# Kernel tuning notes

Hardware: AMD Instinct MI355X
Metric: run time of the kernel (lower is better)

Reference implementation:

```python
import jax, jax.numpy as jnp
import numpy as np
import math

N, CIN, COUT, H, W, K = 8, 192, 192, 64, 64, 1024


def setup_inputs() -> dict:
    key = jax.random.key(0)
    k1, k2, k3, k4, k5 = jax.random.split(key, 5)
    latent = jax.random.normal(k1, (N, CIN, H, W), dtype=jnp.float32)
    # kaiming-uniform-like codebook init
    bound = math.sqrt(6.0 / COUT)
    codebook = jax.random.uniform(k2, (K, COUT), dtype=jnp.float32, minval=-bound, maxval=bound)
    # nn.Linear weights: [out_features, in_features]
    wq = jax.random.normal(k3, (COUT, CIN), dtype=jnp.float32) / math.sqrt(CIN)
    wk = jax.random.normal(k4, (COUT, COUT), dtype=jnp.float32) / math.sqrt(COUT)
    wv = jax.random.normal(k5, (COUT, COUT), dtype=jnp.float32) / math.sqrt(COUT)
    temperature1 = jnp.ones((), dtype=jnp.float32)
    return {"latent": latent, "codebook": codebook, "wq": wq, "wk": wk, "wv": wv,
            "temperature1": temperature1, "temperature": 1}


def reference(latent, codebook, wq, wk, wv, temperature1, temperature):
    # latent: [n, cin, h, w] -> q: [n, h, w, cout]
    q = jnp.einsum('nchw,oc->nhwo', latent, wq)
    k = codebook @ wk.T          # [K, cout]
    v = codebook @ wv.T          # [K, cout]
    scale = math.sqrt(CIN)
    # logit: [n, h, w, K]
    logit = jnp.einsum('nhwd,kd->nhwk', q, k) / scale * temperature1
    trueCode = jnp.argmax(logit, axis=-1)  # [n, h, w]
    # gumbel-softmax, hard=True (straight-through)
    gumbel = jax.random.gumbel(jax.random.key(42), logit.shape, dtype=logit.dtype)
    y_soft = jax.nn.softmax((logit + gumbel) / temperature, axis=-1)
    idx = jnp.argmax(y_soft, axis=-1)
    y_hard = jax.nn.one_hot(idx, K, dtype=logit.dtype)
    sample = y_hard + y_soft - jax.lax.stop_gradient(y_soft)
    # quantized: [n, h, w, cout] -> [n, cout, h, w]
    quantized = jnp.einsum('nhwk,kd->nhwd', sample, v).transpose(0, 3, 1, 2)
    return quantized, trueCode, logit
```

## Files before the change

kernel.cpp:

```cpp
#include <hip/hip_runtime.h>
#include <cstdint>
#include <cstddef>

#define CIN   192
#define COUT  192
#define KCB   1024
#define HWSZ  4096
#define NPIX  32768
#define LOGIT_SCALE_F 13.856406460551018f

#define QCOL0 832

__device__ __forceinline__ void threefry_0_42(uint32_t x0, uint32_t x1,
                                              uint32_t& o0, uint32_t& o1) {
  const uint32_t ks0 = 0u;
  const uint32_t ks1 = 42u;
  const uint32_t ks2 = 0x1BD11BDAu ^ 0u ^ 42u;
  x0 += ks0; x1 += ks1;
#define TFR(r) { x0 += x1; x1 = (x1 << (r)) | (x1 >> (32 - (r))); x1 ^= x0; }
  TFR(13) TFR(15) TFR(26) TFR(6)
  x0 += ks1; x1 += ks2 + 1u;
  TFR(17) TFR(29) TFR(16) TFR(24)
  x0 += ks2; x1 += ks0 + 2u;
  TFR(13) TFR(15) TFR(26) TFR(6)
  x0 += ks0; x1 += ks1 + 3u;
  TFR(17) TFR(29) TFR(16) TFR(24)
  x0 += ks1; x1 += ks2 + 4u;
  TFR(13) TFR(15) TFR(26) TFR(6)
  x0 += ks2; x1 += ks0 + 5u;
#undef TFR
  o0 = x0; o1 = x1;
}

__device__ __forceinline__ float gumbel_from_bits(uint32_t b) {
  float u = __uint_as_float((b >> 9) | 0x3F800000u) - 1.0f;
  u = fmaxf(u, 1.17549435e-38f);
  return -logf(-logf(u));
}

#define FMA16(acc, av, bv) do { \
  acc[0][0]=fmaf(av.x,bv.x,acc[0][0]); acc[0][1]=fmaf(av.x,bv.y,acc[0][1]); \
  acc[0][2]=fmaf(av.x,bv.z,acc[0][2]); acc[0][3]=fmaf(av.x,bv.w,acc[0][3]); \
  acc[1][0]=fmaf(av.y,bv.x,acc[1][0]); acc[1][1]=fmaf(av.y,bv.y,acc[1][1]); \
  acc[1][2]=fmaf(av.y,bv.z,acc[1][2]); acc[1][3]=fmaf(av.y,bv.w,acc[1][3]); \
  acc[2][0]=fmaf(av.z,bv.x,acc[2][0]); acc[2][1]=fmaf(av.z,bv.y,acc[2][1]); \
  acc[2][2]=fmaf(av.z,bv.z,acc[2][2]); acc[2][3]=fmaf(av.z,bv.w,acc[2][3]); \
  acc[3][0]=fmaf(av.w,bv.x,acc[3][0]); acc[3][1]=fmaf(av.w,bv.y,acc[3][1]); \
  acc[3][2]=fmaf(av.w,bv.z,acc[3][2]); acc[3][3]=fmaf(av.w,bv.w,acc[3][3]); \
} while (0)

#define FMA8(accr, a, b0, b1) do { \
  accr[0]=fmaf(a,b0.x,accr[0]); accr[1]=fmaf(a,b0.y,accr[1]); \
  accr[2]=fmaf(a,b0.z,accr[2]); accr[3]=fmaf(a,b0.w,accr[3]); \
  accr[4]=fmaf(a,b1.x,accr[4]); accr[5]=fmaf(a,b1.y,accr[5]); \
  accr[6]=fmaf(a,b1.z,accr[6]); accr[7]=fmaf(a,b1.w,accr[7]); \
} while (0)

__global__ __launch_bounds__(256) void kv_kernel(
    const float* __restrict__ cb, const float* __restrict__ wk,
    const float* __restrict__ wv, float* __restrict__ km, float* __restrict__ vm) {
  __shared__ float sCb[32][68];
  __shared__ float sK[32][68];
  __shared__ float sV[32][68];
  const int tid = threadIdx.x;
  const int j0 = blockIdx.x * 64;
  const int o0 = blockIdx.y * 64;
  const float4* cb4 = reinterpret_cast<const float4*>(cb);
  const float4* wk4 = reinterpret_cast<const float4*>(wk);
  const float4* wv4 = reinterpret_cast<const float4*>(wv);
  const int c4 = tid & 7, rr = tid >> 3;
  const int tp = tid & 15, to = tid >> 4;
  float ak[4][4] = {};
  float av_[4][4] = {};

  for (int ci = 0; ci < 6; ++ci) {
    __syncthreads();
    {
      const int cf = ci * 8 + c4;
#pragma unroll
      for (int pass = 0; pass < 2; ++pass) {
        const int r = rr + pass * 32;
        float4 a = cb4[(size_t)(j0 + r) * 48 + cf];
        float4 b = wk4[(size_t)(o0 + r) * 48 + cf];
        float4 c = wv4[(size_t)(o0 + r) * 48 + cf];
        sCb[4 * c4 + 0][r] = a.x; sCb[4 * c4 + 1][r] = a.y;
        sCb[4 * c4 + 2][r] = a.z; sCb[4 * c4 + 3][r] = a.w;
        sK[4 * c4 + 0][r] = b.x; sK[4 * c4 + 1][r] = b.y;
        sK[4 * c4 + 2][r] = b.z; sK[4 * c4 + 3][r] = b.w;
        sV[4 * c4 + 0][r] = c.x; sV[4 * c4 + 1][r] = c.y;
        sV[4 * c4 + 2][r] = c.z; sV[4 * c4 + 3][r] = c.w;
      }
    }
    __syncthreads();
#pragma unroll
    for (int c = 0; c < 32; ++c) {
      float4 a = *reinterpret_cast<const float4*>(&sCb[c][4 * tp]);
      float4 bk = *reinterpret_cast<const float4*>(&sK[c][4 * to]);
      float4 bv = *reinterpret_cast<const float4*>(&sV[c][4 * to]);
      FMA16(ak, a, bk);
      FMA16(av_, a, bv);
    }
  }
#pragma unroll
  for (int ii = 0; ii < 4; ++ii) {
    float4 w;
    w.x = ak[ii][0]; w.y = ak[ii][1]; w.z = ak[ii][2]; w.w = ak[ii][3];
    *reinterpret_cast<float4*>(km + (size_t)(j0 + 4 * tp + ii) * COUT + o0 + 4 * to) = w;
    float4 v;
    v.x = av_[ii][0]; v.y = av_[ii][1]; v.z = av_[ii][2]; v.w = av_[ii][3];
    *reinterpret_cast<float4*>(vm + (size_t)(j0 + 4 * tp + ii) * COUT + o0 + 4 * to) = v;
  }
}

__global__ __launch_bounds__(256) void q_kernel(
    const float* __restrict__ latent, const float* __restrict__ wq,
    float* __restrict__ logitq) {
  __shared__ float sA[32][68];
  __shared__ float sB[32][68];
  const int tid = threadIdx.x;
  const int p0 = blockIdx.x * 64;
  const int o0 = blockIdx.y * 64;
  const int n = p0 >> 12, hw0 = p0 & 4095;
  const float4* lat4 =
      reinterpret_cast<const float4*>(latent + (size_t)n * (CIN * HWSZ));
  const float4* wq4 = reinterpret_cast<const float4*>(wq);
  const int hw40 = hw0 >> 2;
  const int lf = tid & 15, lr = tid >> 4;
  const int wc4 = tid & 7, wr = tid >> 3;
  const int tp = tid & 15, to = tid >> 4;
  float acc[4][4] = {};

  for (int ci = 0; ci < 6; ++ci) {
    const int c0 = ci * 32;
    __syncthreads();
    {
      float4 l0 = lat4[(size_t)(c0 + lr) * (HWSZ / 4) + hw40 + lf];
      float4 l1 = lat4[(size_t)(c0 + lr + 16) * (HWSZ / 4) + hw40 + lf];
      float4 w0 = wq4[(size_t)(o0 + wr) * 48 + (c0 >> 2) + wc4];
      float4 w1 = wq4[(size_t)(o0 + wr + 32) * 48 + (c0 >> 2) + wc4];
      *reinterpret_cast<float4*>(&sA[lr][4 * lf]) = l0;
      *reinterpret_cast<float4*>(&sA[lr + 16][4 * lf]) = l1;
      sB[4 * wc4 + 0][wr] = w0.x; sB[4 * wc4 + 1][wr] = w0.y;
      sB[4 * wc4 + 2][wr] = w0.z; sB[4 * wc4 + 3][wr] = w0.w;
      sB[4 * wc4 + 0][wr + 32] = w1.x; sB[4 * wc4 + 1][wr + 32] = w1.y;
      sB[4 * wc4 + 2][wr + 32] = w1.z; sB[4 * wc4 + 3][wr + 32] = w1.w;
    }
    __syncthreads();
#pragma unroll
    for (int c = 0; c < 32; ++c) {
      float4 av = *reinterpret_cast<const float4*>(&sA[c][4 * tp]);
      float4 bv = *reinterpret_cast<const float4*>(&sB[c][4 * to]);
      FMA16(acc, av, bv);
    }
  }
#pragma unroll
  for (int ii = 0; ii < 4; ++ii) {
    float4 w;
    w.x = acc[ii][0]; w.y = acc[ii][1]; w.z = acc[ii][2]; w.w = acc[ii][3];
    *reinterpret_cast<float4*>(
        logitq + (size_t)(p0 + 4 * tp + ii) * KCB + QCOL0 + o0 + 4 * to) = w;
  }
}

__global__ __launch_bounds__(256) void logit_kernel(
    const float* __restrict__ km, const float* __restrict__ vm,
    const float* __restrict__ t1p, float* __restrict__ logit_out,
    float* __restrict__ code_out, float* __restrict__ quant_out) {
  __shared__ float aT[CIN][36];
  __shared__ float bT[32][132];
  __shared__ float wLv[32][4];
  __shared__ int   wLi[32][4];
  __shared__ float wSv[32][4];
  __shared__ int   wSi[32][4];
  __shared__ int   sIdx[32];

  const int tid = threadIdx.x;
  const int p0 = blockIdx.x * 32;
  const float t1 = t1p[0];

  for (int i = 0; i < 6; ++i) {
    int flat = tid + i * 256;
    int r = flat / 48, c4 = flat % 48;
    float4 v = reinterpret_cast<const float4*>(
        logit_out + (size_t)(p0 + r) * KCB + QCOL0)[c4];
    aT[c4 * 4 + 0][r] = v.x;
    aT[c4 * 4 + 1][r] = v.y;
    aT[c4 * 4 + 2][r] = v.z;
    aT[c4 * 4 + 3][r] = v.w;
  }

  const int tp = tid & 15;
  const int to = tid >> 4;
  float Lv[2], Sv[2];
  int Li[2], Si[2];
#pragma unroll
  for (int ii = 0; ii < 2; ++ii) {
    Lv[ii] = -INFINITY; Sv[ii] = -INFINITY; Li[ii] = 0; Si[ii] = 0;
  }

  const float4* km4 = reinterpret_cast<const float4*>(km);
  const int sc4 = tid & 7, sjj = tid >> 3;

  for (int jt = 0; jt < 8; ++jt) {
    float acc[2][8] = {};
    for (int ci = 0; ci < 6; ++ci) {
      const int c0 = ci * 32;
      __syncthreads();
      {
#pragma unroll
        for (int pass = 0; pass < 4; ++pass) {
          const int jloc = sjj + pass * 32;
          const int jg = jt * 128 + jloc;
          float4 v = km4[(size_t)jg * 48 + (c0 >> 2) + sc4];
          bT[4 * sc4 + 0][jloc] = v.x; bT[4 * sc4 + 1][jloc] = v.y;
          bT[4 * sc4 + 2][jloc] = v.z; bT[4 * sc4 + 3][jloc] = v.w;
        }
      }
      __syncthreads();
#pragma unroll
      for (int c = 0; c < 32; ++c) {
        float2 a2 = *reinterpret_cast<const float2*>(&aT[c0 + c][2 * tp]);
        float4 b0 = *reinterpret_cast<const float4*>(&bT[c][8 * to]);
        float4 b1 = *reinterpret_cast<const float4*>(&bT[c][8 * to + 4]);
        FMA8(acc[0], a2.x, b0, b1);
        FMA8(acc[1], a2.y, b0, b1);
      }
    }
#pragma unroll
    for (int ii = 0; ii < 2; ++ii) {
      const int p = p0 + 2 * tp + ii;
      const int jb = jt * 128 + 8 * to;
      float lv[8];
#pragma unroll
      for (int k = 0; k < 8; ++k) lv[k] = acc[ii][k] / LOGIT_SCALE_F * t1;
      float4 w0, w1;
      w0.x = lv[0]; w0.y = lv[1]; w0.z = lv[2]; w0.w = lv[3];
      w1.x = lv[4]; w1.y = lv[5]; w1.z = lv[6]; w1.w = lv[7];
      float* lrow = logit_out + (size_t)p * KCB + jb;
      *reinterpret_cast<float4*>(lrow) = w0;
      *reinterpret_cast<float4*>(lrow + 4) = w1;
#pragma unroll
      for (int jj = 0; jj < 8; ++jj) {
        const int jgl = jb + jj;
        const float val = lv[jj];
        if (val > Lv[ii]) { Lv[ii] = val; Li[ii] = jgl; }
        uint32_t b0, b1;
        threefry_0_42(0u, (uint32_t)p * (uint32_t)KCB + (uint32_t)jgl, b0, b1);
        const float s = val + gumbel_from_bits(b0 ^ b1);
        if (s > Sv[ii]) { Sv[ii] = s; Si[ii] = jgl; }
      }
    }
  }

  {
    const int lane = tid & 63;
    const int wvid = tid >> 6;
#pragma unroll
    for (int ii = 0; ii < 2; ++ii) {
      float v = Lv[ii]; int idx = Li[ii];
      float s = Sv[ii]; int sidx = Si[ii];
#pragma unroll
      for (int m = 16; m <= 32; m <<= 1) {
        float v2 = __shfl_xor(v, m); int i2 = __shfl_xor(idx, m);
        if (v2 > v || (v2 == v && i2 < idx)) { v = v2; idx = i2; }
        float s2 = __shfl_xor(s, m); int j2 = __shfl_xor(sidx, m);
        if (s2 > s || (s2 == s && j2 < sidx)) { s = s2; sidx = j2; }
      }
      if (lane < 16) {
        const int r = 2 * tp + ii;
        wLv[r][wvid] = v; wLi[r][wvid] = idx;
        wSv[r][wvid] = s; wSi[r][wvid] = sidx;
      }
    }
  }
  __syncthreads();
  if (tid < 32) {
    const int r = tid;
    float bv = wLv[r][0]; int bi = wLi[r][0];
    float sv = wSv[r][0]; int si = wSi[r][0];
#pragma unroll
    for (int t = 1; t < 4; ++t) {
      float v1 = wLv[r][t]; int i1 = wLi[r][t];
      if (v1 > bv || (v1 == bv && i1 < bi)) { bv = v1; bi = i1; }
      float v2 = wSv[r][t]; int i2 = wSi[r][t];
      if (v2 > sv || (v2 == sv && i2 < si)) { sv = v2; si = i2; }
    }
    code_out[p0 + r] = (float)bi;
    sIdx[r] = si;
  }
  __syncthreads();

  {
    const int l = tid & 31, dg = tid >> 5;
    const int p = p0 + l;
    const int nn = p >> 12, hw = p & 4095;
    const int jv = sIdx[l];
    const float* vrow = vm + (size_t)jv * COUT;
    float* qb = quant_out + (size_t)nn * (COUT * HWSZ) + hw;
#pragma unroll
    for (int it = 0; it < 24; ++it) {
      const int d = it * 8 + dg;
      qb[(size_t)d * HWSZ] = vrow[d];
    }
  }
}

extern "C" void kernel_launch(void* const* d_in, const int* in_sizes, int n_in,
                              void* d_out, int out_size, void* d_ws, size_t ws_size,
                              hipStream_t stream) {
  (void)in_sizes; (void)n_in; (void)out_size; (void)ws_size;
  const float* latent   = (const float*)d_in[0];
  const float* codebook = (const float*)d_in[1];
  const float* wq       = (const float*)d_in[2];
  const float* wk       = (const float*)d_in[3];
  const float* wv       = (const float*)d_in[4];
  const float* t1       = (const float*)d_in[5];

  float* ws = (float*)d_ws;
  float* km = ws;
  float* vm = ws + 196608;

  float* quant = (float*)d_out;
  float* code  = quant + 6291456;
  float* logit = code + 32768;

  kv_kernel<<<dim3(16, 3), dim3(256), 0, stream>>>(codebook, wk, wv, km, vm);
  q_kernel<<<dim3(NPIX / 64, CIN / 64), dim3(256), 0, stream>>>(latent, wq, logit);
  logit_kernel<<<dim3(NPIX / 32), dim3(256), 0, stream>>>(km, vm, t1, logit, code, quant);
}
```

Before: 534.4 us.

## Fuse Q projection into logit GEMM and split gumbel argmax into separate kernel

The Q projection is now computed per 64-pixel block directly into shared memory, so Q no longer round-trips through the logit output buffer, and the logit GEMM tile grows to 64 pixels with 4x8 outputs per thread. The threefry/gumbel argmax and quantized gather move into a new kernel that rereads the logits row-wise, with one wavefront per pixel and full wave shuffle reductions. This removes the intermediate Q store and load and takes the costly RNG work out of the GEMM's register pressure. In exchange, the full logit tensor (128 MB) is read back once more, and each block recomputes its Q tile.

```diff
diff --git a/kernel.cpp b/kernel.cpp
--- a/kernel.cpp
+++ b/kernel.cpp
@@ -8,8 +8,6 @@
 #define HWSZ  4096
 #define NPIX  32768
 #define LOGIT_SCALE_F 13.856406460551018f
-
-#define QCOL0 832
 
 __device__ __forceinline__ void threefry_0_42(uint32_t x0, uint32_t x1,
                                               uint32_t& o0, uint32_t& o1) {
@@ -112,97 +110,67 @@
   }
 }
 
-__global__ __launch_bounds__(256) void q_kernel(
+__global__ __launch_bounds__(256) void qlogit_kernel(
     const float* __restrict__ latent, const float* __restrict__ wq,
-    float* __restrict__ logitq) {
-  __shared__ float sA[32][68];
-  __shared__ float sB[32][68];
+    const float* __restrict__ km, const float* __restrict__ t1p,
+    float* __restrict__ logit_out) {
+  __shared__ __align__(16) float aT[CIN][68];
+  __shared__ __align__(16) float stg[2][32][68];
+  float* bTf = &stg[0][0][0];
+#define BT(r, j) bTf[(r) * 132 + (j)]
+
   const int tid = threadIdx.x;
   const int p0 = blockIdx.x * 64;
-  const int o0 = blockIdx.y * 64;
   const int n = p0 >> 12, hw0 = p0 & 4095;
-  const float4* lat4 =
-      reinterpret_cast<const float4*>(latent + (size_t)n * (CIN * HWSZ));
-  const float4* wq4 = reinterpret_cast<const float4*>(wq);
-  const int hw40 = hw0 >> 2;
-  const int lf = tid & 15, lr = tid >> 4;
-  const int wc4 = tid & 7, wr = tid >> 3;
+  const float t1 = t1p[0];
   const int tp = tid & 15, to = tid >> 4;
-  float acc[4][4] = {};
-
-  for (int ci = 0; ci < 6; ++ci) {
-    const int c0 = ci * 32;
-    __syncthreads();
-    {
-      float4 l0 = lat4[(size_t)(c0 + lr) * (HWSZ / 4) + hw40 + lf];
-      float4 l1 = lat4[(size_t)(c0 + lr + 16) * (HWSZ / 4) + hw40 + lf];
-      float4 w0 = wq4[(size_t)(o0 + wr) * 48 + (c0 >> 2) + wc4];
-      float4 w1 = wq4[(size_t)(o0 + wr + 32) * 48 + (c0 >> 2) + wc4];
-      *reinterpret_cast<float4*>(&sA[lr][4 * lf]) = l0;
-      *reinterpret_cast<float4*>(&sA[lr + 16][4 * lf]) = l1;
-      sB[4 * wc4 + 0][wr] = w0.x; sB[4 * wc4 + 1][wr] = w0.y;
-      sB[4 * wc4 + 2][wr] = w0.z; sB[4 * wc4 + 3][wr] = w0.w;
-      sB[4 * wc4 + 0][wr + 32] = w1.x; sB[4 * wc4 + 1][wr + 32] = w1.y;
-      sB[4 * wc4 + 2][wr + 32] = w1.z; sB[4 * wc4 + 3][wr + 32] = w1.w;
-    }
-    __syncthreads();
-#pragma unroll
-    for (int c = 0; c < 32; ++c) {
-      float4 av = *reinterpret_cast<const float4*>(&sA[c][4 * tp]);
-      float4 bv = *reinterpret_cast<const float4*>(&sB[c][4 * to]);
-      FMA16(acc, av, bv);
-    }
-  }
-#pragma unroll
-  for (int ii = 0; ii < 4; ++ii) {
-    float4 w;
-    w.x = acc[ii][0]; w.y = acc[ii][1]; w.z = acc[ii][2]; w.w = acc[ii][3];
-    *reinterpret_cast<float4*>(
-        logitq + (size_t)(p0 + 4 * tp + ii) * KCB + QCOL0 + o0 + 4 * to) = w;
-  }
-}
-
-__global__ __launch_bounds__(256) void logit_kernel(
-    const float* __restrict__ km, const float* __restrict__ vm,
-    const float* __restrict__ t1p, float* __restrict__ logit_out,
-    float* __restrict__ code_out, float* __restrict__ quant_out) {
-  __shared__ float aT[CIN][36];
-  __shared__ float bT[32][132];
-  __shared__ float wLv[32][4];
-  __shared__ int   wLi[32][4];
-  __shared__ float wSv[32][4];
-  __shared__ int   wSi[32][4];
-  __shared__ int   sIdx[32];
-
-  const int tid = threadIdx.x;
-  const int p0 = blockIdx.x * 32;
-  const float t1 = t1p[0];
-
-  for (int i = 0; i < 6; ++i) {
-    int flat = tid + i * 256;
-    int r = flat / 48, c4 = flat % 48;
-    float4 v = reinterpret_cast<const float4*>(
-        logit_out + (size_t)(p0 + r) * KCB + QCOL0)[c4];
-    aT[c4 * 4 + 0][r] = v.x;
-    aT[c4 * 4 + 1][r] = v.y;
-    aT[c4 * 4 + 2][r] = v.z;
-    aT[c4 * 4 + 3][r] = v.w;
-  }
-
-  const int tp = tid & 15;
-  const int to = tid >> 4;
-  float Lv[2], Sv[2];
-  int Li[2], Si[2];
-#pragma unroll
-  for (int ii = 0; ii < 2; ++ii) {
-    Lv[ii] = -INFINITY; Sv[ii] = -INFINITY; Li[ii] = 0; Si[ii] = 0;
+
+  {
+    const float4* lat4 =
+        reinterpret_cast<const float4*>(latent + (size_t)n * (CIN * HWSZ));
+    const float4* wq4 = reinterpret_cast<const float4*>(wq);
+    const int hw40 = hw0 >> 2;
+    const int lf = tid & 15, lr = tid >> 4;
+    const int wc4 = tid & 7, wr = tid >> 3;
+    for (int ot = 0; ot < 3; ++ot) {
+      const int o0 = ot * 64;
+      float acc[4][4] = {};
+      for (int ci = 0; ci < 6; ++ci) {
+        const int c0 = ci * 32;
+        __syncthreads();
+        {
+          float4 l0 = lat4[(size_t)(c0 + lr) * (HWSZ / 4) + hw40 + lf];
+          float4 l1 = lat4[(size_t)(c0 + lr + 16) * (HWSZ / 4) + hw40 + lf];
+          float4 w0 = wq4[(size_t)(o0 + wr) * 48 + (c0 >> 2) + wc4];
+          float4 w1 = wq4[(size_t)(o0 + wr + 32) * 48 + (c0 >> 2) + wc4];
+          *reinterpret_cast<float4*>(&stg[0][lr][4 * lf]) = l0;
+          *reinterpret_cast<float4*>(&stg[0][lr + 16][4 * lf]) = l1;
+          stg[1][4 * wc4 + 0][wr] = w0.x; stg[1][4 * wc4 + 1][wr] = w0.y;
+          stg[1][4 * wc4 + 2][wr] = w0.z; stg[1][4 * wc4 + 3][wr] = w0.w;
+          stg[1][4 * wc4 + 0][wr + 32] = w1.x; stg[1][4 * wc4 + 1][wr + 32] = w1.y;
+          stg[1][4 * wc4 + 2][wr + 32] = w1.z; stg[1][4 * wc4 + 3][wr + 32] = w1.w;
+        }
+        __syncthreads();
+#pragma unroll
+        for (int c = 0; c < 32; ++c) {
+          float4 av = *reinterpret_cast<const float4*>(&stg[0][c][4 * tp]);
+          float4 bv = *reinterpret_cast<const float4*>(&stg[1][c][4 * to]);
+          FMA16(acc, av, bv);
+        }
+      }
+#pragma unroll
+      for (int ii = 0; ii < 4; ++ii)
+#pragma unroll
+        for (int kk = 0; kk < 4; ++kk)
+          aT[o0 + 4 * to + kk][4 * tp + ii] = acc[ii][kk];
+    }
   }
 
   const float4* km4 = reinterpret_cast<const float4*>(km);
   const int sc4 = tid & 7, sjj = tid >> 3;
 
   for (int jt = 0; jt < 8; ++jt) {
-    float acc[2][8] = {};
+    float acc[4][8] = {};
     for (int ci = 0; ci < 6; ++ci) {
       const int c0 = ci * 32;
       __syncthreads();
@@ -212,94 +180,98 @@
           const int jloc = sjj + pass * 32;
           const int jg = jt * 128 + jloc;
           float4 v = km4[(size_t)jg * 48 + (c0 >> 2) + sc4];
-          bT[4 * sc4 + 0][jloc] = v.x; bT[4 * sc4 + 1][jloc] = v.y;
-          bT[4 * sc4 + 2][jloc] = v.z; bT[4 * sc4 + 3][jloc] = v.w;
+          BT(4 * sc4 + 0, jloc) = v.x; BT(4 * sc4 + 1, jloc) = v.y;
+          BT(4 * sc4 + 2, jloc) = v.z; BT(4 * sc4 + 3, jloc) = v.w;
         }
       }
       __syncthreads();
 #pragma unroll
       for (int c = 0; c < 32; ++c) {
-        float2 a2 = *reinterpret_cast<const float2*>(&aT[c0 + c][2 * tp]);
-        float4 b0 = *reinterpret_cast<const float4*>(&bT[c][8 * to]);
-        float4 b1 = *reinterpret_cast<const float4*>(&bT[c][8 * to + 4]);
-        FMA8(acc[0], a2.x, b0, b1);
-        FMA8(acc[1], a2.y, b0, b1);
-      }
-    }
-#pragma unroll
-    for (int ii = 0; ii < 2; ++ii) {
-      const int p = p0 + 2 * tp + ii;
+        float4 av = *reinterpret_cast<const float4*>(&aT[c0 + c][4 * tp]);
+        float4 b0 = *reinterpret_cast<const float4*>(&BT(c, 8 * to));
+        float4 b1 = *reinterpret_cast<const float4*>(&BT(c, 8 * to + 4));
+        FMA8(acc[0], av.x, b0, b1);
+        FMA8(acc[1], av.y, b0, b1);
+        FMA8(acc[2], av.z, b0, b1);
+        FMA8(acc[3], av.w, b0, b1);
+      }
+    }
+#pragma unroll
+    for (int ii = 0; ii < 4; ++ii) {
+      const int p = p0 + 4 * tp + ii;
       const int jb = jt * 128 + 8 * to;
-      float lv[8];
-#pragma unroll
-      for (int k = 0; k < 8; ++k) lv[k] = acc[ii][k] / LOGIT_SCALE_F * t1;
       float4 w0, w1;
-      w0.x = lv[0]; w0.y = lv[1]; w0.z = lv[2]; w0.w = lv[3];
-      w1.x = lv[4]; w1.y = lv[5]; w1.z = lv[6]; w1.w = lv[7];
+      w0.x = acc[ii][0] / LOGIT_SCALE_F * t1;
+      w0.y = acc[ii][1] / LOGIT_SCALE_F * t1;
+      w0.z = acc[ii][2] / LOGIT_SCALE_F * t1;
+      w0.w = acc[ii][3] / LOGIT_SCALE_F * t1;
+      w1.x = acc[ii][4] / LOGIT_SCALE_F * t1;
+      w1.y = acc[ii][5] / LOGIT_SCALE_F * t1;
+      w1.z = acc[ii][6] / LOGIT_SCALE_F * t1;
+      w1.w = acc[ii][7] / LOGIT_SCALE_F * t1;
       float* lrow = logit_out + (size_t)p * KCB + jb;
       *reinterpret_cast<float4*>(lrow) = w0;
       *reinterpret_cast<float4*>(lrow + 4) = w1;
-#pragma unroll
-      for (int jj = 0; jj < 8; ++jj) {
-        const int jgl = jb + jj;
-        const float val = lv[jj];
-        if (val > Lv[ii]) { Lv[ii] = val; Li[ii] = jgl; }
+    }
+  }
+#undef BT
+}
+
+__global__ __launch_bounds__(256) void gumbel_kernel(
+    const float* __restrict__ logit, const float* __restrict__ vm,
+    float* __restrict__ code_out, float* __restrict__ quant_out) {
+  __shared__ int sIdx[16];
+  const int tid = threadIdx.x;
+  const int p0 = blockIdx.x * 16;
+  const int wv = tid >> 6, lane = tid & 63;
+
+#pragma unroll 1
+  for (int k = 0; k < 4; ++k) {
+    const int p = p0 + wv * 4 + k;
+    const float* lrow = logit + (size_t)p * KCB;
+    float Lv = -INFINITY, Sv = -INFINITY;
+    int Li = 0, Si = 0;
+    const uint32_t pbase = (uint32_t)p * (uint32_t)KCB;
+#pragma unroll
+    for (int ch = 0; ch < 4; ++ch) {
+      const int jb = ch * 256 + 4 * lane;
+      const float4 v = *reinterpret_cast<const float4*>(lrow + jb);
+      const float vals[4] = {v.x, v.y, v.z, v.w};
+#pragma unroll
+      for (int jj = 0; jj < 4; ++jj) {
+        const int j = jb + jj;
+        const float val = vals[jj];
+        if (val > Lv) { Lv = val; Li = j; }
         uint32_t b0, b1;
-        threefry_0_42(0u, (uint32_t)p * (uint32_t)KCB + (uint32_t)jgl, b0, b1);
+        threefry_0_42(0u, pbase + (uint32_t)j, b0, b1);
         const float s = val + gumbel_from_bits(b0 ^ b1);
-        if (s > Sv[ii]) { Sv[ii] = s; Si[ii] = jgl; }
-      }
-    }
-  }
+        if (s > Sv) { Sv = s; Si = j; }
+      }
+    }
+#pragma unroll
+    for (int m = 1; m <= 32; m <<= 1) {
+      const float v2 = __shfl_xor(Lv, m); const int i2 = __shfl_xor(Li, m);
+      if (v2 > Lv || (v2 == Lv && i2 < Li)) { Lv = v2; Li = i2; }
+      const float s2 = __shfl_xor(Sv, m); const int j2 = __shfl_xor(Si, m);
+      if (s2 > Sv || (s2 == Sv && j2 < Si)) { Sv = s2; Si = j2; }
+    }
+    if (lane == 0) {
+      code_out[p] = (float)Li;
+      sIdx[wv * 4 + k] = Si;
+    }
+  }
+  __syncthreads();
 
   {
-    const int lane = tid & 63;
-    const int wvid = tid >> 6;
-#pragma unroll
-    for (int ii = 0; ii < 2; ++ii) {
-      float v = Lv[ii]; int idx = Li[ii];
-      float s = Sv[ii]; int sidx = Si[ii];
-#pragma unroll
-      for (int m = 16; m <= 32; m <<= 1) {
-        float v2 = __shfl_xor(v, m); int i2 = __shfl_xor(idx, m);
-        if (v2 > v || (v2 == v && i2 < idx)) { v = v2; idx = i2; }
-        float s2 = __shfl_xor(s, m); int j2 = __shfl_xor(sidx, m);
-        if (s2 > s || (s2 == s && j2 < sidx)) { s = s2; sidx = j2; }
-      }
-      if (lane < 16) {
-        const int r = 2 * tp + ii;
-        wLv[r][wvid] = v; wLi[r][wvid] = idx;
-        wSv[r][wvid] = s; wSi[r][wvid] = sidx;
-      }
-    }
-  }
-  __syncthreads();
-  if (tid < 32) {
-    const int r = tid;
-    float bv = wLv[r][0]; int bi = wLi[r][0];
-    float sv = wSv[r][0]; int si = wSi[r][0];
-#pragma unroll
-    for (int t = 1; t < 4; ++t) {
-      float v1 = wLv[r][t]; int i1 = wLi[r][t];
-      if (v1 > bv || (v1 == bv && i1 < bi)) { bv = v1; bi = i1; }
-      float v2 = wSv[r][t]; int i2 = wSi[r][t];
-      if (v2 > sv || (v2 == sv && i2 < si)) { sv = v2; si = i2; }
-    }
-    code_out[p0 + r] = (float)bi;
-    sIdx[r] = si;
-  }
-  __syncthreads();
-
-  {
-    const int l = tid & 31, dg = tid >> 5;
-    const int p = p0 + l;
+    const int px = tid & 15, d0 = tid >> 4;
+    const int p = p0 + px;
     const int nn = p >> 12, hw = p & 4095;
-    const int jv = sIdx[l];
+    const int jv = sIdx[px];
     const float* vrow = vm + (size_t)jv * COUT;
     float* qb = quant_out + (size_t)nn * (COUT * HWSZ) + hw;
 #pragma unroll
-    for (int it = 0; it < 24; ++it) {
-      const int d = it * 8 + dg;
+    for (int it = 0; it < 12; ++it) {
+      const int d = it * 16 + d0;
       qb[(size_t)d * HWSZ] = vrow[d];
     }
   }
@@ -325,6 +297,6 @@
   float* logit = code + 32768;
 
   kv_kernel<<<dim3(16, 3), dim3(256), 0, stream>>>(codebook, wk, wv, km, vm);
-  q_kernel<<<dim3(NPIX / 64, CIN / 64), dim3(256), 0, stream>>>(latent, wq, logit);
-  logit_kernel<<<dim3(NPIX / 32), dim3(256), 0, stream>>>(km, vm, t1, logit, code, quant);
-}
+  qlogit_kernel<<<dim3(NPIX / 64), dim3(256), 0, stream>>>(latent, wq, km, t1, logit);
+  gumbel_kernel<<<dim3(NPIX / 16), dim3(256), 0, stream>>>(logit, vm, code, quant);
+}
```

Result: slower. 615.7 us (+15.2%).

## Enlarge logit GEMM register tile to 4x16 and retile q GEMM over all outputs

Applied to the files above, without the earlier changes.

The logit kernel now processes 64 pixels per block with a 4x16 per-thread accumulator over 256-code tiles. It streams q slices through shared memory per channel chunk instead of holding the full transposed q block, which raises arithmetic intensity per shared load and halves codebook-key reloads across blocks. The q kernel computes all 192 outputs for 32 pixels per block with a 2x12 tile, so each latent tile is read once rather than three times. The larger accumulators increase register pressure, hence the occupancy hint of 2 on the logit kernel, which may cause spills. Fewer blocks means less parallelism per wave.

```diff
diff --git a/kernel.cpp b/kernel.cpp
--- a/kernel.cpp
+++ b/kernel.cpp
@@ -49,13 +49,6 @@
   acc[3][2]=fmaf(av.w,bv.z,acc[3][2]); acc[3][3]=fmaf(av.w,bv.w,acc[3][3]); \
 } while (0)
 
-#define FMA8(accr, a, b0, b1) do { \
-  accr[0]=fmaf(a,b0.x,accr[0]); accr[1]=fmaf(a,b0.y,accr[1]); \
-  accr[2]=fmaf(a,b0.z,accr[2]); accr[3]=fmaf(a,b0.w,accr[3]); \
-  accr[4]=fmaf(a,b1.x,accr[4]); accr[5]=fmaf(a,b1.y,accr[5]); \
-  accr[6]=fmaf(a,b1.z,accr[6]); accr[7]=fmaf(a,b1.w,accr[7]); \
-} while (0)
-
 __global__ __launch_bounds__(256) void kv_kernel(
     const float* __restrict__ cb, const float* __restrict__ wk,
     const float* __restrict__ wv, float* __restrict__ km, float* __restrict__ vm) {
@@ -115,139 +108,156 @@
 __global__ __launch_bounds__(256) void q_kernel(
     const float* __restrict__ latent, const float* __restrict__ wq,
     float* __restrict__ logitq) {
-  __shared__ float sA[32][68];
-  __shared__ float sB[32][68];
+  __shared__ float sA[32][36];
+  __shared__ float sB[32][196];
   const int tid = threadIdx.x;
-  const int p0 = blockIdx.x * 64;
-  const int o0 = blockIdx.y * 64;
+  const int p0 = blockIdx.x * 32;
   const int n = p0 >> 12, hw0 = p0 & 4095;
   const float4* lat4 =
       reinterpret_cast<const float4*>(latent + (size_t)n * (CIN * HWSZ));
   const float4* wq4 = reinterpret_cast<const float4*>(wq);
   const int hw40 = hw0 >> 2;
-  const int lf = tid & 15, lr = tid >> 4;
-  const int wc4 = tid & 7, wr = tid >> 3;
+  const int af = tid & 7, ar = tid >> 3;
+  const int wc8 = tid & 7, wr = tid >> 3;
   const int tp = tid & 15, to = tid >> 4;
-  float acc[4][4] = {};
+  float acc[2][12] = {};
 
   for (int ci = 0; ci < 6; ++ci) {
     const int c0 = ci * 32;
     __syncthreads();
     {
-      float4 l0 = lat4[(size_t)(c0 + lr) * (HWSZ / 4) + hw40 + lf];
-      float4 l1 = lat4[(size_t)(c0 + lr + 16) * (HWSZ / 4) + hw40 + lf];
-      float4 w0 = wq4[(size_t)(o0 + wr) * 48 + (c0 >> 2) + wc4];
-      float4 w1 = wq4[(size_t)(o0 + wr + 32) * 48 + (c0 >> 2) + wc4];
-      *reinterpret_cast<float4*>(&sA[lr][4 * lf]) = l0;
-      *reinterpret_cast<float4*>(&sA[lr + 16][4 * lf]) = l1;
-      sB[4 * wc4 + 0][wr] = w0.x; sB[4 * wc4 + 1][wr] = w0.y;
-      sB[4 * wc4 + 2][wr] = w0.z; sB[4 * wc4 + 3][wr] = w0.w;
-      sB[4 * wc4 + 0][wr + 32] = w1.x; sB[4 * wc4 + 1][wr + 32] = w1.y;
-      sB[4 * wc4 + 2][wr + 32] = w1.z; sB[4 * wc4 + 3][wr + 32] = w1.w;
+      float4 l = lat4[(size_t)(c0 + ar) * (HWSZ / 4) + hw40 + af];
+      *reinterpret_cast<float4*>(&sA[ar][4 * af]) = l;
+#pragma unroll
+      for (int pass = 0; pass < 6; ++pass) {
+        const int o = wr + pass * 32;
+        float4 w = wq4[(size_t)o * 48 + (c0 >> 2) + wc8];
+        sB[4 * wc8 + 0][o] = w.x; sB[4 * wc8 + 1][o] = w.y;
+        sB[4 * wc8 + 2][o] = w.z; sB[4 * wc8 + 3][o] = w.w;
+      }
     }
     __syncthreads();
 #pragma unroll
     for (int c = 0; c < 32; ++c) {
-      float4 av = *reinterpret_cast<const float4*>(&sA[c][4 * tp]);
-      float4 bv = *reinterpret_cast<const float4*>(&sB[c][4 * to]);
-      FMA16(acc, av, bv);
-    }
-  }
-#pragma unroll
-  for (int ii = 0; ii < 4; ++ii) {
-    float4 w;
-    w.x = acc[ii][0]; w.y = acc[ii][1]; w.z = acc[ii][2]; w.w = acc[ii][3];
-    *reinterpret_cast<float4*>(
-        logitq + (size_t)(p0 + 4 * tp + ii) * KCB + QCOL0 + o0 + 4 * to) = w;
-  }
-}
-
-__global__ __launch_bounds__(256) void logit_kernel(
+      float2 a2 = *reinterpret_cast<const float2*>(&sA[c][2 * tp]);
+      float4 b0 = *reinterpret_cast<const float4*>(&sB[c][12 * to]);
+      float4 b1 = *reinterpret_cast<const float4*>(&sB[c][12 * to + 4]);
+      float4 b2 = *reinterpret_cast<const float4*>(&sB[c][12 * to + 8]);
+      const float av[2] = {a2.x, a2.y};
+      const float bv[12] = {b0.x, b0.y, b0.z, b0.w, b1.x, b1.y,
+                            b1.z, b1.w, b2.x, b2.y, b2.z, b2.w};
+#pragma unroll
+      for (int i = 0; i < 2; ++i)
+#pragma unroll
+        for (int k = 0; k < 12; ++k)
+          acc[i][k] = fmaf(av[i], bv[k], acc[i][k]);
+    }
+  }
+#pragma unroll
+  for (int i = 0; i < 2; ++i) {
+    const int p = p0 + 2 * tp + i;
+    float* qr = logitq + (size_t)p * KCB + QCOL0 + 12 * to;
+    float4 w0, w1, w2;
+    w0.x = acc[i][0]; w0.y = acc[i][1]; w0.z = acc[i][2]; w0.w = acc[i][3];
+    w1.x = acc[i][4]; w1.y = acc[i][5]; w1.z = acc[i][6]; w1.w = acc[i][7];
+    w2.x = acc[i][8]; w2.y = acc[i][9]; w2.z = acc[i][10]; w2.w = acc[i][11];
+    *reinterpret_cast<float4*>(qr) = w0;
+    *reinterpret_cast<float4*>(qr + 4) = w1;
+    *reinterpret_cast<float4*>(qr + 8) = w2;
+  }
+}
+
+__global__ __launch_bounds__(256, 2) void logit_kernel(
     const float* __restrict__ km, const float* __restrict__ vm,
     const float* __restrict__ t1p, float* __restrict__ logit_out,
     float* __restrict__ code_out, float* __restrict__ quant_out) {
-  __shared__ float aT[CIN][36];
-  __shared__ float bT[32][132];
-  __shared__ float wLv[32][4];
-  __shared__ int   wLi[32][4];
-  __shared__ float wSv[32][4];
-  __shared__ int   wSi[32][4];
-  __shared__ int   sIdx[32];
+  __shared__ float sA[32][68];
+  __shared__ float sB[32][260];
+  __shared__ float wLv[64][4];
+  __shared__ int   wLi[64][4];
+  __shared__ float wSv[64][4];
+  __shared__ int   wSi[64][4];
+  __shared__ int   sIdx[64];
 
   const int tid = threadIdx.x;
-  const int p0 = blockIdx.x * 32;
+  const int p0 = blockIdx.x * 64;
   const float t1 = t1p[0];
-
-  for (int i = 0; i < 6; ++i) {
-    int flat = tid + i * 256;
-    int r = flat / 48, c4 = flat % 48;
-    float4 v = reinterpret_cast<const float4*>(
-        logit_out + (size_t)(p0 + r) * KCB + QCOL0)[c4];
-    aT[c4 * 4 + 0][r] = v.x;
-    aT[c4 * 4 + 1][r] = v.y;
-    aT[c4 * 4 + 2][r] = v.z;
-    aT[c4 * 4 + 3][r] = v.w;
-  }
-
   const int tp = tid & 15;
   const int to = tid >> 4;
-  float Lv[2], Sv[2];
-  int Li[2], Si[2];
-#pragma unroll
-  for (int ii = 0; ii < 2; ++ii) {
+  const int qc8 = tid & 7, qr = tid >> 3;
+  const float4* km4 = reinterpret_cast<const float4*>(km);
+
+  float Lv[4], Sv[4];
+  int Li[4], Si[4];
+#pragma unroll
+  for (int ii = 0; ii < 4; ++ii) {
     Lv[ii] = -INFINITY; Sv[ii] = -INFINITY; Li[ii] = 0; Si[ii] = 0;
   }
 
-  const float4* km4 = reinterpret_cast<const float4*>(km);
-  const int sc4 = tid & 7, sjj = tid >> 3;
-
-  for (int jt = 0; jt < 8; ++jt) {
-    float acc[2][8] = {};
+  for (int jt = 0; jt < 4; ++jt) {
+    float acc[4][16] = {};
     for (int ci = 0; ci < 6; ++ci) {
       const int c0 = ci * 32;
       __syncthreads();
       {
 #pragma unroll
-        for (int pass = 0; pass < 4; ++pass) {
-          const int jloc = sjj + pass * 32;
-          const int jg = jt * 128 + jloc;
-          float4 v = km4[(size_t)jg * 48 + (c0 >> 2) + sc4];
-          bT[4 * sc4 + 0][jloc] = v.x; bT[4 * sc4 + 1][jloc] = v.y;
-          bT[4 * sc4 + 2][jloc] = v.z; bT[4 * sc4 + 3][jloc] = v.w;
+        for (int pass = 0; pass < 2; ++pass) {
+          const int r = qr + pass * 32;
+          float4 a = *reinterpret_cast<const float4*>(
+              logit_out + (size_t)(p0 + r) * KCB + QCOL0 + c0 + 4 * qc8);
+          sA[4 * qc8 + 0][r] = a.x; sA[4 * qc8 + 1][r] = a.y;
+          sA[4 * qc8 + 2][r] = a.z; sA[4 * qc8 + 3][r] = a.w;
         }
+#pragma unroll
+        for (int pass = 0; pass < 8; ++pass) {
+          const int j = qr + pass * 32;
+          float4 b = km4[(size_t)(jt * 256 + j) * 48 + (c0 >> 2) + qc8];
+          sB[4 * qc8 + 0][j] = b.x; sB[4 * qc8 + 1][j] = b.y;
+          sB[4 * qc8 + 2][j] = b.z; sB[4 * qc8 + 3][j] = b.w;
+        }
       }
       __syncthreads();
 #pragma unroll
       for (int c = 0; c < 32; ++c) {
-        float2 a2 = *reinterpret_cast<const float2*>(&aT[c0 + c][2 * tp]);
-        float4 b0 = *reinterpret_cast<const float4*>(&bT[c][8 * to]);
-        float4 b1 = *reinterpret_cast<const float4*>(&bT[c][8 * to + 4]);
-        FMA8(acc[0], a2.x, b0, b1);
-        FMA8(acc[1], a2.y, b0, b1);
-      }
-    }
-#pragma unroll
-    for (int ii = 0; ii < 2; ++ii) {
-      const int p = p0 + 2 * tp + ii;
-      const int jb = jt * 128 + 8 * to;
-      float lv[8];
-#pragma unroll
-      for (int k = 0; k < 8; ++k) lv[k] = acc[ii][k] / LOGIT_SCALE_F * t1;
-      float4 w0, w1;
-      w0.x = lv[0]; w0.y = lv[1]; w0.z = lv[2]; w0.w = lv[3];
-      w1.x = lv[4]; w1.y = lv[5]; w1.z = lv[6]; w1.w = lv[7];
+        float4 a = *reinterpret_cast<const float4*>(&sA[c][4 * tp]);
+        float4 b0 = *reinterpret_cast<const float4*>(&sB[c][16 * to]);
+        float4 b1 = *reinterpret_cast<const float4*>(&sB[c][16 * to + 4]);
+        float4 b2 = *reinterpret_cast<const float4*>(&sB[c][16 * to + 8]);
+        float4 b3 = *reinterpret_cast<const float4*>(&sB[c][16 * to + 12]);
+        const float av[4] = {a.x, a.y, a.z, a.w};
+        const float bv[16] = {b0.x, b0.y, b0.z, b0.w, b1.x, b1.y, b1.z, b1.w,
+                              b2.x, b2.y, b2.z, b2.w, b3.x, b3.y, b3.z, b3.w};
+#pragma unroll
+        for (int i = 0; i < 4; ++i)
+#pragma unroll
+          for (int k = 0; k < 16; ++k)
+            acc[i][k] = fmaf(av[i], bv[k], acc[i][k]);
+      }
+    }
+#pragma unroll
+    for (int i = 0; i < 4; ++i) {
+      const int p = p0 + 4 * tp + i;
+      const int jb = jt * 256 + 16 * to;
+      float lv[16];
+#pragma unroll
+      for (int k = 0; k < 16; ++k) lv[k] = acc[i][k] / LOGIT_SCALE_F * t1;
       float* lrow = logit_out + (size_t)p * KCB + jb;
-      *reinterpret_cast<float4*>(lrow) = w0;
-      *reinterpret_cast<float4*>(lrow + 4) = w1;
-#pragma unroll
-      for (int jj = 0; jj < 8; ++jj) {
-        const int jgl = jb + jj;
-        const float val = lv[jj];
-        if (val > Lv[ii]) { Lv[ii] = val; Li[ii] = jgl; }
+#pragma unroll
+      for (int m = 0; m < 4; ++m) {
+        float4 w;
+        w.x = lv[4 * m + 0]; w.y = lv[4 * m + 1];
+        w.z = lv[4 * m + 2]; w.w = lv[4 * m + 3];
+        *reinterpret_cast<float4*>(lrow + 4 * m) = w;
+      }
+      const uint32_t pb = (uint32_t)p * (uint32_t)KCB + (uint32_t)jb;
+#pragma unroll
+      for (int k = 0; k < 16; ++k) {
+        const float val = lv[k];
+        if (val > Lv[i]) { Lv[i] = val; Li[i] = jb + k; }
         uint32_t b0, b1;
-        threefry_0_42(0u, (uint32_t)p * (uint32_t)KCB + (uint32_t)jgl, b0, b1);
+        threefry_0_42(0u, pb + (uint32_t)k, b0, b1);
         const float s = val + gumbel_from_bits(b0 ^ b1);
-        if (s > Sv[ii]) { Sv[ii] = s; Si[ii] = jgl; }
+        if (s > Sv[i]) { Sv[i] = s; Si[i] = jb + k; }
       }
     }
   }
@@ -256,7 +266,7 @@
     const int lane = tid & 63;
     const int wvid = tid >> 6;
 #pragma unroll
-    for (int ii = 0; ii < 2; ++ii) {
+    for (int ii = 0; ii < 4; ++ii) {
       float v = Lv[ii]; int idx = Li[ii];
       float s = Sv[ii]; int sidx = Si[ii];
 #pragma unroll
@@ -267,14 +277,14 @@
         if (s2 > s || (s2 == s && j2 < sidx)) { s = s2; sidx = j2; }
       }
       if (lane < 16) {
-        const int r = 2 * tp + ii;
+        const int r = 4 * tp + ii;
         wLv[r][wvid] = v; wLi[r][wvid] = idx;
         wSv[r][wvid] = s; wSi[r][wvid] = sidx;
       }
     }
   }
   __syncthreads();
-  if (tid < 32) {
+  if (tid < 64) {
     const int r = tid;
     float bv = wLv[r][0]; int bi = wLi[r][0];
     float sv = wSv[r][0]; int si = wSi[r][0];
@@ -291,15 +301,15 @@
   __syncthreads();
 
   {
-    const int l = tid & 31, dg = tid >> 5;
+    const int l = tid & 63, dg = tid >> 6;
     const int p = p0 + l;
     const int nn = p >> 12, hw = p & 4095;
     const int jv = sIdx[l];
     const float* vrow = vm + (size_t)jv * COUT;
     float* qb = quant_out + (size_t)nn * (COUT * HWSZ) + hw;
 #pragma unroll
-    for (int it = 0; it < 24; ++it) {
-      const int d = it * 8 + dg;
+    for (int it = 0; it < 48; ++it) {
+      const int d = it * 4 + dg;
       qb[(size_t)d * HWSZ] = vrow[d];
     }
   }
@@ -325,6 +335,6 @@
   float* logit = code + 32768;
 
   kv_kernel<<<dim3(16, 3), dim3(256), 0, stream>>>(codebook, wk, wv, km, vm);
-  q_kernel<<<dim3(NPIX / 64, CIN / 64), dim3(256), 0, stream>>>(latent, wq, logit);
-  logit_kernel<<<dim3(NPIX / 32), dim3(256), 0, stream>>>(km, vm, t1, logit, code, quant);
-}
+  q_kernel<<<dim3(NPIX / 32), dim3(256), 0, stream>>>(latent, wq, logit);
+  logit_kernel<<<dim3(NPIX / 64), dim3(256), 0, stream>>>(km, vm, t1, logit, code, quant);
+}
```

Result: faster. 462.1 us (-13.5%).
